# Optimization experiments

Measured on AMD Instinct MI355X. Metric: run time of the kernel, lower is better.

The kernel has to match this reference:

```python
import jax, jax.numpy as jnp
import numpy as np
from jax import lax

B_, N, C, NH, KB = 4096, 64, 192, 6, 8
WH = WW = 8  # win_size
HD = C // NH
KS = 5  # depthwise kernel size (distance=2)


def _rel_pos_index(wh, ww, k_bound):
    ch = np.arange(wh); cw = np.arange(ww)
    coords = np.stack(np.meshgrid(ch, cw, indexing='ij'))  # (2, wh, ww)
    cf = coords.reshape(2, -1)
    rel = cf[:, :, None] - cf[:, None, :]
    rel = np.clip(rel, -(k_bound - 1), k_bound - 1).transpose(1, 2, 0).astype(np.int32)
    rel[..., 0] += k_bound - 1
    rel[..., 1] += k_bound - 1
    rel[..., 0] *= 2 * k_bound - 1
    return rel.sum(-1)  # (N, N) indices into (2k-1)^2 table


def setup_inputs() -> dict:
    key = jax.random.key(0)
    ks = jax.random.split(key, 12)
    s = 0.02
    x = jax.random.normal(ks[0], (B_, N, C), dtype=jnp.float32)
    wq = jax.random.normal(ks[1], (C, C), dtype=jnp.float32) * s
    bq = jnp.zeros((C,), dtype=jnp.float32)
    wkv = jax.random.normal(ks[2], (C, 3 * C), dtype=jnp.float32) * s
    bkv = jnp.zeros((3 * C,), dtype=jnp.float32)
    rpb_table = jax.random.normal(ks[3], ((2 * KB - 1) * (2 * KB - 1), NH), dtype=jnp.float32) * s
    rel_index = jnp.asarray(_rel_pos_index(WH, WW, KB), dtype=jnp.int32)
    dw_w = jax.random.normal(ks[4], (C, 1, KS, KS), dtype=jnp.float32) * s   # depthwise, groups=C
    dw_b = jnp.zeros((C,), dtype=jnp.float32)
    pw_w = jax.random.normal(ks[5], (C, C // NH, 1, 1), dtype=jnp.float32) * s  # 1x1, groups=NH
    pw_b = jnp.zeros((C,), dtype=jnp.float32)
    proj_w = jax.random.normal(ks[6], (C, C), dtype=jnp.float32) * s
    proj_b = jnp.zeros((C,), dtype=jnp.float32)
    return dict(x=x, wq=wq, bq=bq, wkv=wkv, bkv=bkv, rpb_table=rpb_table,
                rel_index=rel_index, dw_w=dw_w, dw_b=dw_b, pw_w=pw_w, pw_b=pw_b,
                proj_w=proj_w, proj_b=proj_b)


def reference(x, wq, bq, wkv, bkv, rpb_table, rel_index, dw_w, dw_b, pw_w, pw_b, proj_w, proj_b):
    B, Nn, Cc = x.shape
    H = int(round(Nn ** 0.5))
    scale = (Cc // NH) ** -0.5
    # QKV projections
    q = (x @ wq + bq).reshape(B, Nn, NH, HD).transpose(0, 2, 1, 3)          # (B, nH, N, hd)
    kv = (x @ wkv + bkv).reshape(B, Nn, 3, NH, HD)
    k = kv[:, :, 0].transpose(0, 2, 1, 3)                                    # (B, nH, N, hd)
    v = kv[:, :, 1].transpose(0, 2, 1, 3)                                    # (B, nH, N, hd)
    v_r = kv[:, :, 2].transpose(0, 2, 3, 1).reshape(B, Cc, H, H)             # (B, C, H, H)
    # attention scores + relative position bias
    attn = jnp.einsum('bhnd,bhmd->bhnm', q * scale, k)
    bias = rpb_table[rel_index.reshape(-1)].reshape(Nn, Nn, NH).transpose(2, 0, 1)  # (nH, N, N)
    attn = jax.nn.softmax(attn + bias[None], axis=-1)
    # positional conv branch: depthwise 5x5 then grouped 1x1
    dn = ('NCHW', 'OIHW', 'NCHW')
    p = lax.conv_general_dilated(v_r, dw_w, (1, 1), 'SAME', dimension_numbers=dn,
                                 feature_group_count=Cc) + dw_b[None, :, None, None]
    p = lax.conv_general_dilated(p, pw_w, (1, 1), 'SAME', dimension_numbers=dn,
                                 feature_group_count=NH) + pw_b[None, :, None, None]
    position = p.reshape(B, Cc, Nn).transpose(0, 2, 1)                       # (B, N, C)
    out = jnp.einsum('bhnm,bhmd->bnhd', attn, v).reshape(B, Nn, Cc) + position
    return out @ proj_w + proj_b
```

## Files before the change

kernel.cpp:

```cpp
#include <hip/hip_runtime.h>

typedef _Float16 half8 __attribute__((ext_vector_type(8)));
typedef _Float16 half4 __attribute__((ext_vector_type(4)));
typedef _Float16 half2 __attribute__((ext_vector_type(2)));
typedef float floatx4 __attribute__((ext_vector_type(4)));

union H8 { half8 h8; half4 h4[2]; half2 h2[4]; int i[4]; };

__device__ __forceinline__ int packh2(float a, float b) {
    union { _Float16 h[2]; int i; } u;
    u.h[0] = (_Float16)a; u.h[1] = (_Float16)b;
    return u.i;
}

__device__ __forceinline__ half8 gather8(int idxA, int idxB, bool sel,
                                         int A0, int A1, int B0, int B1) {
    int a0 = __builtin_amdgcn_ds_bpermute(idxA, A0);
    int b0 = __builtin_amdgcn_ds_bpermute(idxA, B0);
    int a1 = __builtin_amdgcn_ds_bpermute(idxA, A1);
    int b1 = __builtin_amdgcn_ds_bpermute(idxA, B1);
    int a2 = __builtin_amdgcn_ds_bpermute(idxB, A0);
    int b2 = __builtin_amdgcn_ds_bpermute(idxB, B0);
    int a3 = __builtin_amdgcn_ds_bpermute(idxB, A1);
    int b3 = __builtin_amdgcn_ds_bpermute(idxB, B1);
    H8 u;
    u.i[0] = sel ? b0 : a0;
    u.i[1] = sel ? b1 : a1;
    u.i[2] = sel ? b2 : a2;
    u.i[3] = sel ? b3 : a3;
    return u.h8;
}


__global__ __launch_bounds__(512) void prep_kernel(
    const float* __restrict__ wq, const float* __restrict__ wkv,
    const float* __restrict__ proj_w, const float* __restrict__ rpb,
    const int* __restrict__ rel,
    const float* __restrict__ dw_w, const float* __restrict__ dw_b,
    const float* __restrict__ pw_w,
    _Float16* __restrict__ WtF, _Float16* __restrict__ PtF,
    float* __restrict__ biasF, _Float16* __restrict__ dwF,
    _Float16* __restrict__ dwbF, _Float16* __restrict__ pwF)
{
    int idx = blockIdx.x * 512 + threadIdx.x;
    if (idx < 147456) {
        int j = idx & 7, lane = (idx >> 3) & 63, t = idx >> 9;
        int ks = t % 6, nt = t / 6;
        int k = ks * 32 + (lane >> 4) * 8 + j;
        int n = nt * 16 + (lane & 15);
        float v = (n < 192) ? wq[k * 192 + n] : wkv[k * 576 + (n - 192)];
        WtF[idx] = (_Float16)v;
    } else if (idx < 184320) {
        int i2 = idx - 147456;
        int j = i2 & 7, lane = (i2 >> 3) & 63, t = i2 >> 9;
        int ks = t % 6, nt = t / 6;
        int k = ks * 32 + (lane >> 4) * 8 + j;
        int n = nt * 16 + (lane & 15);
        PtF[i2] = (_Float16)proj_w[k * 192 + n];
    } else if (idx < 208896) {
        int i2 = idx - 184320;
        int r = i2 & 3, lane = (i2 >> 2) & 63, t = i2 >> 8;
        int ntq = t & 3, mt = (t >> 2) & 3, h = t >> 4;
        int m = mt * 16 + (lane >> 4) * 4 + r;
        int n = ntq * 16 + (lane & 15);
        biasF[i2] = rpb[rel[n * 64 + m] * 6 + h];
    } else if (idx < 213696) {
        int i2 = idx - 208896;
        int j = i2 & 7, t = i2 >> 3;
        int tap = t % 25, gk = t / 25;
        int c = (gk >> 2) * 32 + (gk & 3) * 8 + j;
        dwF[i2] = (_Float16)dw_w[c * 25 + tap];
    } else if (idx < 213888) {
        int i2 = idx - 213696;
        int j = i2 & 7, gk = i2 >> 3;
        int c = (gk >> 2) * 32 + (gk & 3) * 8 + j;
        dwbF[i2] = (_Float16)dw_b[c];
    } else if (idx < 220032) {
        int i2 = idx - 213888;
        int j = i2 & 7, lane = (i2 >> 3) & 63, t = i2 >> 9;
        int ntc = t & 1, g = t >> 1;
        int oc = g * 32 + ntc * 16 + (lane & 15);
        int ic = (lane >> 4) * 8 + j;
        pwF[i2] = (_Float16)pw_w[oc * 32 + ic];
    }
}


#define XO   0
#define VRO  12800
#define SCR  25600
#define ZO   40192

__global__ __launch_bounds__(384, 3) void wa_main(
    const float* __restrict__ xg,
    const float* __restrict__ bq, const float* __restrict__ bkv,
    const float* __restrict__ proj_bg, const float* __restrict__ pw_b,
    const _Float16* __restrict__ WtF, const _Float16* __restrict__ PtF,
    const float* __restrict__ biasF,
    const _Float16* __restrict__ dwF, const _Float16* __restrict__ dwbF,
    const _Float16* __restrict__ pwF,
    float* __restrict__ outg)
{
    extern __shared__ unsigned char smem[];
    _Float16* sHalf = (_Float16*)smem;

    const int b    = blockIdx.x;
    const int tid  = threadIdx.x;
    const int lane = tid & 63;
    const int h    = tid >> 6;
    const int mrow = lane & 15;
    const int kq   = lane >> 4;
    const float scale = 0.17677669529663687f;
    _Float16* sS = sHalf + SCR + h * 2432;

    const float* xb = xg + (size_t)b * 12288;
    #pragma unroll
    for (int it = 0; it < 8; ++it) {
        int f4  = it * 384 + tid;
        int row = f4 / 48;
        int col = (f4 % 48) * 4;
        float4 v = ((const float4*)xb)[f4];
        half4 p;
        p[0] = (_Float16)v.x; p[1] = (_Float16)v.y;
        p[2] = (_Float16)v.z; p[3] = (_Float16)v.w;
        *(half4*)(sHalf + XO + row * 200 + col) = p;
    }
    if (tid < 8) sHalf[ZO + tid] = (_Float16)0.0f;
    __syncthreads();

    #pragma unroll
    for (int t = 0; t < 2; ++t) {
        int nt = 36 + 2 * h + t;
        half8 bf[6];
        #pragma unroll
        for (int ks = 0; ks < 6; ++ks)
            bf[ks] = ((const half8*)WtF)[(nt * 6 + ks) * 64 + lane];
        float4 b4 = *(const float4*)(bkv + nt * 16 - 192 + kq * 4);
        floatx4 binit = {b4.x, b4.y, b4.z, b4.w};
        #pragma unroll
        for (int mt4 = 0; mt4 < 4; ++mt4) {
            floatx4 acc = binit;
            #pragma unroll
            for (int ks = 0; ks < 6; ++ks) {
                half8 af = *(const half8*)(sHalf + XO + (mt4 * 16 + mrow) * 200 + ks * 32 + kq * 8);
                acc = __builtin_amdgcn_mfma_f32_16x16x32_f16(bf[ks], af, acc, 0, 0, 0);
            }
            union { int i2[2]; half4 h4; } u;
            u.i2[0] = packh2(acc[0], acc[1]);
            u.i2[1] = packh2(acc[2], acc[3]);
            *(half4*)(sHalf + VRO + (mt4 * 16 + mrow) * 200 + h * 32 + t * 16 + kq * 4) = u.h4;
        }
    }

    half8 aK[4], bQ[4];
    #pragma unroll
    for (int qk = 0; qk < 2; ++qk) {
        #pragma unroll
        for (int hf = 0; hf < 2; ++hf) {
            #pragma unroll
            for (int t = 0; t < 2; ++t) {
                int nt = (qk == 0 ? 12 : 0) + 2 * h + t;
                half8 bf[6];
                #pragma unroll
                for (int ks = 0; ks < 6; ++ks)
                    bf[ks] = ((const half8*)WtF)[(nt * 6 + ks) * 64 + lane];
                const float* bptr = (qk == 0) ? (bkv + nt * 16 - 192) : (bq + nt * 16);
                float4 b4 = *(const float4*)(bptr + kq * 4);
                floatx4 binit = {b4.x, b4.y, b4.z, b4.w};
                #pragma unroll
                for (int mt2 = 0; mt2 < 2; ++mt2) {
                    int mt4 = hf * 2 + mt2;
                    floatx4 acc = binit;
                    #pragma unroll
                    for (int ks = 0; ks < 6; ++ks) {
                        half8 af = *(const half8*)(sHalf + XO + (mt4 * 16 + mrow) * 200 + ks * 32 + kq * 8);
                        acc = __builtin_amdgcn_mfma_f32_16x16x32_f16(bf[ks], af, acc, 0, 0, 0);
                    }
                    if (qk == 1) {
                        acc[0] *= scale; acc[1] *= scale; acc[2] *= scale; acc[3] *= scale;
                    }
                    union { int i2[2]; half4 h4; } u;
                    u.i2[0] = packh2(acc[0], acc[1]);
                    u.i2[1] = packh2(acc[2], acc[3]);
                    *(half4*)(sS + (mt2 * 16 + mrow) * 40 + t * 16 + kq * 4) = u.h4;
                }
            }
            #pragma unroll
            for (int q2 = 0; q2 < 2; ++q2) {
                half8 f = *(const half8*)(sS + (q2 * 16 + mrow) * 40 + kq * 8);
                if (qk == 0) aK[hf * 2 + q2] = f;
                else         bQ[hf * 2 + q2] = f;
            }
        }
    }

    #pragma unroll
    for (int t = 0; t < 2; ++t) {
        int nt = 24 + 2 * h + t;
        half8 bf[6];
        #pragma unroll
        for (int ks = 0; ks < 6; ++ks)
            bf[ks] = ((const half8*)WtF)[(nt * 6 + ks) * 64 + lane];
        float bv = bkv[nt * 16 - 192 + mrow];
        #pragma unroll
        for (int mt = 0; mt < 4; ++mt) {
            floatx4 acc = {bv, bv, bv, bv};
            #pragma unroll
            for (int ks = 0; ks < 6; ++ks) {
                half8 af = *(const half8*)(sHalf + XO + (mt * 16 + mrow) * 200 + ks * 32 + kq * 8);
                acc = __builtin_amdgcn_mfma_f32_16x16x32_f16(af, bf[ks], acc, 0, 0, 0);
            }
            union { int i2[2]; half4 h4; } u;
            u.i2[0] = packh2(acc[0], acc[1]);
            u.i2[1] = packh2(acc[2], acc[3]);
            *(half4*)(sS + mrow * 152 + t * 72 + mt * 16 + kq * 4) = u.h4;
        }
    }

    const int cb32 = h * 32 + kq * 8;
    const half8* dwFp = (const half8*)dwF + (h * 4 + kq) * 25;
    H8 bini; bini.h8 = ((const half8*)dwbF)[h * 4 + kq];
    half2 cacc[4][4];
    #pragma unroll
    for (int mt = 0; mt < 4; ++mt)
        #pragma unroll
        for (int p = 0; p < 4; ++p) cacc[mt][p] = bini.h2[p];

    int ni[4], nj[4];
    #pragma unroll
    for (int mt = 0; mt < 4; ++mt) { int n = mt * 16 + mrow; ni[mt] = n >> 3; nj[mt] = n & 7; }

    #pragma unroll 5
    for (int t = 0; t < 25; ++t) {
        H8 w; w.h8 = dwFp[t];
        int di = t / 5 - 2, dj = t % 5 - 2;
        #pragma unroll
        for (int mt = 0; mt < 4; ++mt) {
            int ii = ni[mt] + di, jj = nj[mt] + dj;
            bool ok = ((unsigned)ii < 8u) & ((unsigned)jj < 8u);
            int off = ok ? (VRO + ((ii << 3) + jj) * 200 + cb32) : ZO;
            H8 d; d.h8 = *(const half8*)(sHalf + off);
            #pragma unroll
            for (int p = 0; p < 4; ++p) cacc[mt][p] += d.h2[p] * w.h2[p];
        }
    }
    half8 dwA[4];
    #pragma unroll
    for (int mt = 0; mt < 4; ++mt) {
        H8 u;
        #pragma unroll
        for (int p = 0; p < 4; ++p) u.h2[p] = cacc[mt][p];
        dwA[mt] = u.h8;
    }

    floatx4 accPV[4][2];
    #pragma unroll
    for (int ntc = 0; ntc < 2; ++ntc) {
        half8 pwB = ((const half8*)pwF)[(h * 2 + ntc) * 64 + lane];
        float4 pb4 = *(const float4*)(pw_b + h * 32 + ntc * 16 + kq * 4);
        #pragma unroll
        for (int mt = 0; mt < 4; ++mt) {
            floatx4 acc = {pb4.x, pb4.y, pb4.z, pb4.w};
            accPV[mt][ntc] = __builtin_amdgcn_mfma_f32_16x16x32_f16(pwB, dwA[mt], acc, 0, 0, 0);
        }
    }

    const int idxA = ((kq & 1) * 32 + mrow) * 4;
    const int idxB = idxA + 64;
    const bool sel = (kq >= 2);

    #pragma unroll
    for (int hf = 0; hf < 2; ++hf) {
        floatx4 stt[4][2];
        #pragma unroll
        for (int mtk = 0; mtk < 4; ++mtk)
            #pragma unroll
            for (int q2 = 0; q2 < 2; ++q2) {
                floatx4 bb = *(const floatx4*)(biasF + (((h * 4 + mtk) * 4 + hf * 2 + q2) * 64 + lane) * 4);
                stt[mtk][q2] = __builtin_amdgcn_mfma_f32_16x16x32_f16(aK[mtk], bQ[hf * 2 + q2], bb, 0, 0, 0);
            }

        #pragma unroll
        for (int q2 = 0; q2 < 2; ++q2) {
            float mx = stt[0][q2][0];
            #pragma unroll
            for (int mtk = 0; mtk < 4; ++mtk)
                #pragma unroll
                for (int r = 0; r < 4; ++r) mx = fmaxf(mx, stt[mtk][q2][r]);
            mx = fmaxf(mx, __shfl_xor(mx, 16));
            mx = fmaxf(mx, __shfl_xor(mx, 32));
            float sm = 0.0f;
            #pragma unroll
            for (int mtk = 0; mtk < 4; ++mtk)
                #pragma unroll
                for (int r = 0; r < 4; ++r) {
                    float e = __expf(stt[mtk][q2][r] - mx);
                    stt[mtk][q2][r] = e;
                    sm += e;
                }
            sm += __shfl_xor(sm, 16);
            sm += __shfl_xor(sm, 32);
            float inv = 1.0f / sm;
            #pragma unroll
            for (int mtk = 0; mtk < 4; ++mtk)
                #pragma unroll
                for (int r = 0; r < 4; ++r) stt[mtk][q2][r] *= inv;
        }

        int pk[4][2][2];
        #pragma unroll
        for (int mtk = 0; mtk < 4; ++mtk)
            #pragma unroll
            for (int q2 = 0; q2 < 2; ++q2) {
                pk[mtk][q2][0] = packh2(stt[mtk][q2][0], stt[mtk][q2][1]);
                pk[mtk][q2][1] = packh2(stt[mtk][q2][2], stt[mtk][q2][3]);
            }
        #pragma unroll
        for (int q2 = 0; q2 < 2; ++q2) {
            int mtq = hf * 2 + q2;
            #pragma unroll
            for (int ks2 = 0; ks2 < 2; ++ks2) {
                half8 aP = gather8(idxA, idxB, sel,
                                   pk[2 * ks2][q2][0],     pk[2 * ks2][q2][1],
                                   pk[2 * ks2 + 1][q2][0], pk[2 * ks2 + 1][q2][1]);
                #pragma unroll
                for (int ntd = 0; ntd < 2; ++ntd) {
                    half8 bVv = *(const half8*)(sS + mrow * 152 + ntd * 72 + ks2 * 32 + kq * 8);
                    accPV[mtq][ntd] = __builtin_amdgcn_mfma_f32_16x16x32_f16(
                        bVv, aP, accPV[mtq][ntd], 0, 0, 0);
                }
            }
        }
    }

    #pragma unroll
    for (int mtq = 0; mtq < 4; ++mtq)
        #pragma unroll
        for (int ntd = 0; ntd < 2; ++ntd) {
            floatx4 o = accPV[mtq][ntd];
            union { int i2[2]; half4 h4; } u;
            u.i2[0] = packh2(o[0], o[1]);
            u.i2[1] = packh2(o[2], o[3]);
            *(half4*)(sHalf + VRO + (mtq * 16 + mrow) * 200 + h * 32 + ntd * 16 + kq * 4) = u.h4;
        }
    __syncthreads();

    float* og = outg + (size_t)b * 12288;
    #pragma unroll
    for (int tnt = 0; tnt < 2; ++tnt) {
        int nt = 2 * h + tnt;
        half8 bf[6];
        #pragma unroll
        for (int ks = 0; ks < 6; ++ks)
            bf[ks] = ((const half8*)PtF)[(nt * 6 + ks) * 64 + lane];
        float bv = proj_bg[nt * 16 + mrow];
        #pragma unroll
        for (int mt = 0; mt < 4; ++mt) {
            floatx4 acc = {bv, bv, bv, bv};
            #pragma unroll
            for (int ks = 0; ks < 6; ++ks) {
                half8 af = *(const half8*)(sHalf + VRO + (mt * 16 + mrow) * 200 + ks * 32 + kq * 8);
                acc = __builtin_amdgcn_mfma_f32_16x16x32_f16(af, bf[ks], acc, 0, 0, 0);
            }
            int m0 = mt * 16 + kq * 4;
            #pragma unroll
            for (int r = 0; r < 4; ++r)
                og[(m0 + r) * 192 + nt * 16 + mrow] = acc[r];
        }
    }
}

extern "C" void kernel_launch(void* const* d_in, const int* in_sizes, int n_in,
                              void* d_out, int out_size, void* d_ws, size_t ws_size,
                              hipStream_t stream) {
    (void)in_sizes; (void)n_in; (void)out_size; (void)ws_size;
    const float* x      = (const float*)d_in[0];
    const float* wq     = (const float*)d_in[1];
    const float* bq     = (const float*)d_in[2];
    const float* wkv    = (const float*)d_in[3];
    const float* bkv    = (const float*)d_in[4];
    const float* rpb    = (const float*)d_in[5];
    const int*   rel    = (const int*)d_in[6];
    const float* dw_w   = (const float*)d_in[7];
    const float* dw_b   = (const float*)d_in[8];
    const float* pw_w   = (const float*)d_in[9];
    const float* pw_b   = (const float*)d_in[10];
    const float* proj_w = (const float*)d_in[11];
    const float* proj_b = (const float*)d_in[12];

    _Float16* WtF  = (_Float16*)d_ws;
    _Float16* PtF  = (_Float16*)((char*)d_ws + 294912);
    float*    biasF= (float*)((char*)d_ws + 368640);
    _Float16* dwF  = (_Float16*)((char*)d_ws + 466944);
    _Float16* dwbF = (_Float16*)((char*)d_ws + 476544);
    _Float16* pwF  = (_Float16*)((char*)d_ws + 476928);

    prep_kernel<<<430, 512, 0, stream>>>(wq, wkv, proj_w, rpb, rel, dw_w, dw_b, pw_w,
                                         WtF, PtF, biasF, dwF, dwbF, pwF);
    wa_main<<<4096, 384, 80400, stream>>>(x, bq, bkv, proj_b, pw_b,
                                          WtF, PtF, biasF, dwF, dwbF, pwF,
                                          (float*)d_out);
}
```

Baseline: 627.0 us.

## Stage positional conv output in LDS and process attention one query tile at a time

The grouped 1x1 conv result is no longer held as 32 float registers across the attention phase. It is rounded to fp16 and written to shared memory, then reloaded as the initial accumulator for each query tile. The softmax/PV loop now handles one 16-query tile per iteration instead of two, which shrinks live register state. The launch bound drops from 3 to 2 blocks per SM. This trades register pressure for extra LDS traffic and an extra fp16 rounding of the position term, and it may reduce occupancy.

```diff
diff --git a/kernel.cpp b/kernel.cpp
--- a/kernel.cpp
+++ b/kernel.cpp
@@ -11,6 +11,13 @@
     union { _Float16 h[2]; int i; } u;
     u.h[0] = (_Float16)a; u.h[1] = (_Float16)b;
     return u.i;
+}
+
+__device__ __forceinline__ floatx4 unpack4(int lo, int hi) {
+    union { int i; _Float16 h[2]; } a, b;
+    a.i = lo; b.i = hi;
+    floatx4 r = {(float)a.h[0], (float)a.h[1], (float)b.h[0], (float)b.h[1]};
+    return r;
 }
 
 __device__ __forceinline__ half8 gather8(int idxA, int idxB, bool sel,
@@ -91,7 +98,7 @@
 #define SCR  25600
 #define ZO   40192
 
-__global__ __launch_bounds__(384, 3) void wa_main(
+__global__ __launch_bounds__(384, 2) void wa_main(
     const float* __restrict__ xg,
     const float* __restrict__ bq, const float* __restrict__ bkv,
     const float* __restrict__ proj_bg, const float* __restrict__ pw_b,
@@ -253,7 +260,6 @@
         dwA[mt] = u.h8;
     }
 
-    floatx4 accPV[4][2];
     #pragma unroll
     for (int ntc = 0; ntc < 2; ++ntc) {
         half8 pwB = ((const half8*)pwF)[(h * 2 + ntc) * 64 + lane];
@@ -261,7 +267,11 @@
         #pragma unroll
         for (int mt = 0; mt < 4; ++mt) {
             floatx4 acc = {pb4.x, pb4.y, pb4.z, pb4.w};
-            accPV[mt][ntc] = __builtin_amdgcn_mfma_f32_16x16x32_f16(pwB, dwA[mt], acc, 0, 0, 0);
+            acc = __builtin_amdgcn_mfma_f32_16x16x32_f16(pwB, dwA[mt], acc, 0, 0, 0);
+            union { int i2[2]; half4 h4; } u;
+            u.i2[0] = packh2(acc[0], acc[1]);
+            u.i2[1] = packh2(acc[2], acc[3]);
+            *(half4*)(sHalf + VRO + (mt * 16 + mrow) * 200 + h * 32 + ntc * 16 + kq * 4) = u.h4;
         }
     }
 
@@ -270,79 +280,70 @@
     const bool sel = (kq >= 2);
 
     #pragma unroll
-    for (int hf = 0; hf < 2; ++hf) {
-        floatx4 stt[4][2];
+    for (int ntq = 0; ntq < 4; ++ntq) {
+        floatx4 stt[4];
+        #pragma unroll
+        for (int mtk = 0; mtk < 4; ++mtk) {
+            floatx4 bb = *(const floatx4*)(biasF + (((h * 4 + mtk) * 4 + ntq) * 64 + lane) * 4);
+            stt[mtk] = __builtin_amdgcn_mfma_f32_16x16x32_f16(aK[mtk], bQ[ntq], bb, 0, 0, 0);
+        }
+
+        float mx = stt[0][0];
         #pragma unroll
         for (int mtk = 0; mtk < 4; ++mtk)
             #pragma unroll
-            for (int q2 = 0; q2 < 2; ++q2) {
-                floatx4 bb = *(const floatx4*)(biasF + (((h * 4 + mtk) * 4 + hf * 2 + q2) * 64 + lane) * 4);
-                stt[mtk][q2] = __builtin_amdgcn_mfma_f32_16x16x32_f16(aK[mtk], bQ[hf * 2 + q2], bb, 0, 0, 0);
-            }
-
-        #pragma unroll
-        for (int q2 = 0; q2 < 2; ++q2) {
-            float mx = stt[0][q2][0];
-            #pragma unroll
-            for (int mtk = 0; mtk < 4; ++mtk)
-                #pragma unroll
-                for (int r = 0; r < 4; ++r) mx = fmaxf(mx, stt[mtk][q2][r]);
-            mx = fmaxf(mx, __shfl_xor(mx, 16));
-            mx = fmaxf(mx, __shfl_xor(mx, 32));
-            float sm = 0.0f;
-            #pragma unroll
-            for (int mtk = 0; mtk < 4; ++mtk)
-                #pragma unroll
-                for (int r = 0; r < 4; ++r) {
-                    float e = __expf(stt[mtk][q2][r] - mx);
-                    stt[mtk][q2][r] = e;
-                    sm += e;
-                }
-            sm += __shfl_xor(sm, 16);
-            sm += __shfl_xor(sm, 32);
-            float inv = 1.0f / sm;
-            #pragma unroll
-            for (int mtk = 0; mtk < 4; ++mtk)
-                #pragma unroll
-                for (int r = 0; r < 4; ++r) stt[mtk][q2][r] *= inv;
-        }
-
-        int pk[4][2][2];
+            for (int r = 0; r < 4; ++r) mx = fmaxf(mx, stt[mtk][r]);
+        mx = fmaxf(mx, __shfl_xor(mx, 16));
+        mx = fmaxf(mx, __shfl_xor(mx, 32));
+        float sm = 0.0f;
         #pragma unroll
         for (int mtk = 0; mtk < 4; ++mtk)
             #pragma unroll
-            for (int q2 = 0; q2 < 2; ++q2) {
-                pk[mtk][q2][0] = packh2(stt[mtk][q2][0], stt[mtk][q2][1]);
-                pk[mtk][q2][1] = packh2(stt[mtk][q2][2], stt[mtk][q2][3]);
-            }
-        #pragma unroll
-        for (int q2 = 0; q2 < 2; ++q2) {
-            int mtq = hf * 2 + q2;
-            #pragma unroll
-            for (int ks2 = 0; ks2 < 2; ++ks2) {
-                half8 aP = gather8(idxA, idxB, sel,
-                                   pk[2 * ks2][q2][0],     pk[2 * ks2][q2][1],
-                                   pk[2 * ks2 + 1][q2][0], pk[2 * ks2 + 1][q2][1]);
-                #pragma unroll
-                for (int ntd = 0; ntd < 2; ++ntd) {
-                    half8 bVv = *(const half8*)(sS + mrow * 152 + ntd * 72 + ks2 * 32 + kq * 8);
-                    accPV[mtq][ntd] = __builtin_amdgcn_mfma_f32_16x16x32_f16(
-                        bVv, aP, accPV[mtq][ntd], 0, 0, 0);
-                }
-            }
-        }
-    }
-
-    #pragma unroll
-    for (int mtq = 0; mtq < 4; ++mtq)
+            for (int r = 0; r < 4; ++r) {
+                float e = __expf(stt[mtk][r] - mx);
+                stt[mtk][r] = e;
+                sm += e;
+            }
+        sm += __shfl_xor(sm, 16);
+        sm += __shfl_xor(sm, 32);
+        float inv = 1.0f / sm;
+
+        int pk[4][2];
+        #pragma unroll
+        for (int mtk = 0; mtk < 4; ++mtk) {
+            pk[mtk][0] = packh2(stt[mtk][0] * inv, stt[mtk][1] * inv);
+            pk[mtk][1] = packh2(stt[mtk][2] * inv, stt[mtk][3] * inv);
+        }
+
+        floatx4 acc[2];
         #pragma unroll
         for (int ntd = 0; ntd < 2; ++ntd) {
-            floatx4 o = accPV[mtq][ntd];
+            union { half4 h4; int i2[2]; } u;
+            u.h4 = *(const half4*)(sHalf + VRO + (ntq * 16 + mrow) * 200 + h * 32 + ntd * 16 + kq * 4);
+            acc[ntd] = unpack4(u.i2[0], u.i2[1]);
+        }
+
+        #pragma unroll
+        for (int ks2 = 0; ks2 < 2; ++ks2) {
+            half8 aP = gather8(idxA, idxB, sel,
+                               pk[2 * ks2][0],     pk[2 * ks2][1],
+                               pk[2 * ks2 + 1][0], pk[2 * ks2 + 1][1]);
+            #pragma unroll
+            for (int ntd = 0; ntd < 2; ++ntd) {
+                half8 bVv = *(const half8*)(sS + mrow * 152 + ntd * 72 + ks2 * 32 + kq * 8);
+                acc[ntd] = __builtin_amdgcn_mfma_f32_16x16x32_f16(bVv, aP, acc[ntd], 0, 0, 0);
+            }
+        }
+
+        #pragma unroll
+        for (int ntd = 0; ntd < 2; ++ntd) {
+            floatx4 o = acc[ntd];
             union { int i2[2]; half4 h4; } u;
             u.i2[0] = packh2(o[0], o[1]);
             u.i2[1] = packh2(o[2], o[3]);
-            *(half4*)(sHalf + VRO + (mtq * 16 + mrow) * 200 + h * 32 + ntd * 16 + kq * 4) = u.h4;
-        }
+            *(half4*)(sHalf + VRO + (ntq * 16 + mrow) * 200 + h * 32 + ntd * 16 + kq * 4) = u.h4;
+        }
+    }
     __syncthreads();
 
     float* og = outg + (size_t)b * 12288;
```

New measurement: 591.0 us. -5.7%, faster.
